# Kernel tuning notes

Hardware: AMD Instinct MI355X
Metric: run time of the kernel (lower is better)

## Reference

```python
import jax, jax.numpy as jnp
import numpy as np

N = 4096  # n == m: vector length and circulant size


def setup_inputs() -> dict:
    key = jax.random.key(0)
    ks = jax.random.split(key, 6)
    return {
        "key": jax.random.normal(ks[0], (N,), dtype=jnp.float32),
        "input_x": jax.random.normal(ks[1], (N,), dtype=jnp.float32),
        "key_matrix1": jax.random.normal(ks[2], (N, N), dtype=jnp.float32),
        "input_o1": jax.random.normal(ks[3], (N,), dtype=jnp.float32),
        "key_matrix2": jax.random.normal(ks[4], (N, N), dtype=jnp.float32),
        "input_o2": jax.random.normal(ks[5], (N,), dtype=jnp.float32),
    }


def reference(key, input_x, key_matrix1, input_o1, key_matrix2, input_o2):
    # Original loop: key_current_j[k] = key[(k - j) % m]  (a rolled copy of key),
    # result[j] = dot(key_current_j, input_x), then per-j correction:
    #   redun1 = (km1 @ key_current_j)[j]
    #   redun2 = sum_{i != j} (km1 @ key_current_j)[i] * input_o1[i]
    # and likewise redun3/redun4 with km2/input_o2; finally
    #   result[j] = (result[j] - redun2 - redun4) / redun1, returning (result, last redun3).
    n = input_x.shape[0]
    m = key.shape[0]
    # Circulant gather: K[j, k] = key[(k - j) % m], shape (n, m)
    idx = (jnp.arange(m)[None, :] - jnp.arange(n)[:, None]) % m
    K = key[idx]

    base = K @ input_x                                   # result before correction, (n,)

    # Diagonals of R = K @ km.T without forming R: d[j] = dot(K[j], km[j])
    d1 = jnp.einsum("jk,jk->j", K, key_matrix1)          # redun1 per j
    d2 = jnp.einsum("jk,jk->j", K, key_matrix2)          # redun3 per j

    # R @ o = (K @ km.T) @ o = K @ (km.T @ o): O(n^2) instead of O(n^3)
    r2 = K @ (key_matrix1.T @ input_o1) - d1 * input_o1  # redun2 per j (index j excluded)
    r4 = K @ (key_matrix2.T @ input_o2) - d2 * input_o2  # redun4 per j

    result = (base - r2 - r4) / d1
    redun3 = d2[-1]  # value from the last loop iteration j = n-1
    return result, redun3
```

## Files before the change

### kernel.cpp

```cpp
#include <hip/hip_runtime.h>

#define N 4096
#define MASK 4095

__device__ __forceinline__ float fold(float u, float v, int m) {
    const bool hi = (threadIdx.x & m) != 0;
    const float t = hi ? u : v;
    const float s = __shfl_xor(t, m, 64);
    return (hi ? v : u) + s;
}

__device__ __forceinline__ float greduce4(float g0, float g1, float g2, float g3) {
    float c1 = fold(g0, g1, 32);
    float c2 = fold(g2, g3, 32);
    float e  = fold(c1, c2, 16);
    e += __shfl_xor(e, 8, 64);
    e += __shfl_xor(e, 4, 64);
    e += __shfl_xor(e, 2, 64);
    e += __shfl_xor(e, 1, 64);
    return e;
}

__global__ __launch_bounds__(256) void k1_fused(
    const float* __restrict__ key,
    const float* __restrict__ km1, const float* __restrict__ km2,
    const float* __restrict__ o1, const float* __restrict__ o2,
    float* __restrict__ tpart1, float* __restrict__ tpart2,
    float* __restrict__ dpart1, float* __restrict__ dpart2)
{
    __shared__ float skey[544];
    const int t = threadIdx.x;
    const int b = blockIdx.x;
    const int rc = b >> 3;
    const int cc = b & 7;
    const int j0 = rc * 16;
    const int c0 = cc * 512;
    const int base = c0 - j0 - 15;

    for (int i = t; i < 527; i += 256)
        skey[i + (i >> 5)] = key[(base + i) & MASK];
    __syncthreads();

    float w[17];
    #pragma unroll
    for (int c = 0; c < 17; ++c) {
        const int idx = 2 * t + c;
        w[c] = skey[idx + (idx >> 5)];
    }

    const float2* q1 = (const float2*)(km1 + (size_t)j0 * N + c0);
    const float2* q2 = (const float2*)(km2 + (size_t)j0 * N + c0);

    float2 La[2][4], Lb[2][4];
    #pragma unroll
    for (int i = 0; i < 4; ++i) La[0][i] = q1[(size_t)i * 2048 + t];
    #pragma unroll
    for (int i = 0; i < 4; ++i) Lb[0][i] = q2[(size_t)i * 2048 + t];

    float tp1x = 0.f, tp1y = 0.f, tp2x = 0.f, tp2y = 0.f;
    float rd1[4], rd2[4];

    #pragma unroll
    for (int rb = 0; rb < 4; ++rb) {
        const int cur = rb & 1, nxt = cur ^ 1;
        if (rb < 3) {
            #pragma unroll
            for (int i = 0; i < 4; ++i) La[nxt][i] = q1[(size_t)((rb + 1) * 4 + i) * 2048 + t];
            #pragma unroll
            for (int i = 0; i < 4; ++i) Lb[nxt][i] = q2[(size_t)((rb + 1) * 4 + i) * 2048 + t];
        }
        float dpa[4], dpb[4];
        #pragma unroll
        for (int rr = 0; rr < 4; ++rr) {
            const int r = rb * 4 + rr;
            const float k0 = w[15 - r], k1v = w[16 - r];
            dpa[rr] = k0 * La[cur][rr].x + k1v * La[cur][rr].y;
            dpb[rr] = k0 * Lb[cur][rr].x + k1v * Lb[cur][rr].y;
            const float oa = o1[j0 + r], ob = o2[j0 + r];
            tp1x += oa * La[cur][rr].x; tp1y += oa * La[cur][rr].y;
            tp2x += ob * Lb[cur][rr].x; tp2y += ob * Lb[cur][rr].y;
        }
        rd1[rb] = greduce4(dpa[0], dpa[1], dpa[2], dpa[3]);
        rd2[rb] = greduce4(dpb[0], dpb[1], dpb[2], dpb[3]);
    }

    const int lane = t & 63, wave = t >> 6, sg = lane >> 4;
    const int off = (0x3120 >> (sg * 4)) & 0xF;
    if ((lane & 15) == 0) {
        #pragma unroll
        for (int qq = 0; qq < 4; ++qq) {
            dpart1[(size_t)(j0 + 4 * qq + off) * 32 + cc * 4 + wave] = rd1[qq];
            dpart2[(size_t)(j0 + 4 * qq + off) * 32 + cc * 4 + wave] = rd2[qq];
        }
    }

    ((float2*)(tpart1 + (size_t)rc * N + c0))[t] = make_float2(tp1x, tp1y);
    ((float2*)(tpart2 + (size_t)rc * N + c0))[t] = make_float2(tp2x, tp2y);
}

__global__ __launch_bounds__(256) void k2_reduce(
    const float* __restrict__ tpart1, const float* __restrict__ tpart2,
    const float* __restrict__ dpart1, const float* __restrict__ dpart2,
    float* __restrict__ t1, float* __restrict__ t2,
    float* __restrict__ d1, float* __restrict__ d2)
{
    __shared__ float sdata[256];
    const int b = blockIdx.x;
    const int t = threadIdx.x;

    if (b < 256) {
        const float* src = (b < 128) ? tpart1 : tpart2;
        float* dst       = (b < 128) ? t1 : t2;
        const int colbase = (b & 127) * 32;
        const int col = t & 31;
        const int sg = t >> 5;
        float a0 = 0.f, a1 = 0.f, a2 = 0.f, a3 = 0.f;
        #pragma unroll 4
        for (int k = 0; k < 32; k += 4) {
            a0 += src[(size_t)(sg + 8 * (k + 0)) * N + colbase + col];
            a1 += src[(size_t)(sg + 8 * (k + 1)) * N + colbase + col];
            a2 += src[(size_t)(sg + 8 * (k + 2)) * N + colbase + col];
            a3 += src[(size_t)(sg + 8 * (k + 3)) * N + colbase + col];
        }
        sdata[t] = (a0 + a1) + (a2 + a3);
        __syncthreads();
        if (t < 32) {
            float s = 0.f;
            #pragma unroll
            for (int i = 0; i < 8; ++i) s += sdata[i * 32 + t];
            dst[colbase + t] = s;
        }
    } else {
        const int db = b - 256;
        const float* src = (db < 512) ? dpart1 : dpart2;
        float* dst       = (db < 512) ? d1 : d2;
        const int rowbase = (db & 511) * 8;
        const int row = rowbase + (t >> 5);
        const int s = t & 31;
        float v = src[(size_t)row * 32 + s];
        #pragma unroll
        for (int off = 16; off > 0; off >>= 1) v += __shfl_down(v, off, 32);
        if (s == 0) dst[row] = v;
    }
}

__global__ __launch_bounds__(256) void k3_final(
    const float* __restrict__ key, const float* __restrict__ x,
    const float* __restrict__ t1, const float* __restrict__ t2,
    const float* __restrict__ d1, const float* __restrict__ d2,
    const float* __restrict__ o1, const float* __restrict__ o2,
    float* __restrict__ out)
{
    __shared__ float skey[4096 + 128];
    __shared__ float sred[48];
    const int t = threadIdx.x;
    const int j0 = blockIdx.x * 4;

    #pragma unroll
    for (int q = 0; q < 16; ++q) {
        const int idx = q * 256 + t;
        skey[idx + (idx >> 5)] = key[idx];
    }
    __syncthreads();

    float acc[4][3];
    #pragma unroll
    for (int r = 0; r < 4; ++r)
        #pragma unroll
        for (int v = 0; v < 3; ++v) acc[r][v] = 0.f;

    #pragma unroll
    for (int q = 0; q < 4; ++q) {
        const int k0 = q * 1024 + 4 * t;
        const float4 xv = *(const float4*)(x + k0);
        const float4 u1 = *(const float4*)(t1 + k0);
        const float4 u2 = *(const float4*)(t2 + k0);
        float kw[7];
        #pragma unroll
        for (int i = 0; i < 7; ++i) {
            const int widx = (k0 - j0 - 3 + i) & MASK;
            kw[i] = skey[widx + (widx >> 5)];
        }
        #pragma unroll
        for (int r = 0; r < 4; ++r) {
            const float kv0 = kw[3 - r], kv1 = kw[4 - r], kv2 = kw[5 - r], kv3 = kw[6 - r];
            acc[r][0] += kv0 * xv.x + kv1 * xv.y + kv2 * xv.z + kv3 * xv.w;
            acc[r][1] += kv0 * u1.x + kv1 * u1.y + kv2 * u1.z + kv3 * u1.w;
            acc[r][2] += kv0 * u2.x + kv1 * u2.y + kv2 * u2.z + kv3 * u2.w;
        }
    }

    float rv[3];
    #pragma unroll
    for (int v = 0; v < 3; ++v)
        rv[v] = greduce4(acc[0][v], acc[1][v], acc[2][v], acc[3][v]);

    const int lane = t & 63, wave = t >> 6, sg = lane >> 4;
    const int off = (0x3120 >> (sg * 4)) & 0xF;
    if ((lane & 15) == 0) {
        #pragma unroll
        for (int v = 0; v < 3; ++v) sred[wave * 12 + v * 4 + off] = rv[v];
    }
    __syncthreads();

    if (t < 4) {
        const int j = j0 + t;
        float vb = 0.f, v1 = 0.f, v2 = 0.f;
        #pragma unroll
        for (int wv = 0; wv < 4; ++wv) {
            vb += sred[wv * 12 + 0 + t];
            v1 += sred[wv * 12 + 4 + t];
            v2 += sred[wv * 12 + 8 + t];
        }
        const float dd1 = d1[j], dd2 = d2[j];
        const float r2 = v1 - dd1 * o1[j];
        const float r4 = v2 - dd2 * o2[j];
        out[j] = (vb - r2 - r4) / dd1;
        if (j == N - 1) out[N] = dd2;
    }
}

extern "C" void kernel_launch(void* const* d_in, const int* in_sizes, int n_in,
                              void* d_out, int out_size, void* d_ws, size_t ws_size,
                              hipStream_t stream) {
    const float* key = (const float*)d_in[0];
    const float* x   = (const float*)d_in[1];
    const float* km1 = (const float*)d_in[2];
    const float* o1  = (const float*)d_in[3];
    const float* km2 = (const float*)d_in[4];
    const float* o2  = (const float*)d_in[5];
    float* out = (float*)d_out;

    float* ws = (float*)d_ws;
    float* tpart1 = ws;
    float* tpart2 = tpart1 + (size_t)256 * N;
    float* dpart1 = tpart2 + (size_t)256 * N;
    float* dpart2 = dpart1 + (size_t)N * 32;
    float* t1     = dpart2 + (size_t)N * 32;
    float* t2     = t1 + N;
    float* d1     = t2 + N;
    float* d2     = d1 + N;

    hipLaunchKernelGGL(k1_fused, dim3(2048), dim3(256), 0, stream,
                       key, km1, km2, o1, o2, tpart1, tpart2, dpart1, dpart2);
    hipLaunchKernelGGL(k2_reduce, dim3(1280), dim3(256), 0, stream,
                       tpart1, tpart2, dpart1, dpart2, t1, t2, d1, d2);
    hipLaunchKernelGGL(k3_final, dim3(1024), dim3(256), 0, stream,
                       key, x, t1, t2, d1, d2, o1, o2, out);
}
```

Before: 35.27 us.

## Give each k1 block full rows with 1024 threads and float4 loads

The first kernel now launches 256 blocks of 1024 threads. Each block covers 16 full rows of both matrices using float4 loads, replacing 2048 blocks of 256 threads that each handled a 16x512 tile. The full key vector is staged in shared memory per block, and the per-row diagonal dot products are reduced with a 32-lane xor shuffle, writing 32 partials per row so the layout matches the existing reduce kernel. This widens memory transactions and cuts the block count, but uses fewer blocks on a large GPU, issues more shuffles per row, and adds a bigger shared-memory load per block.

```diff
diff --git a/kernel.cpp b/kernel.cpp
--- a/kernel.cpp
+++ b/kernel.cpp
@@ -2,6 +2,15 @@
 
 #define N 4096
 #define MASK 4095
+
+__device__ __forceinline__ float red32(float v) {
+    v += __shfl_xor(v, 1, 64);
+    v += __shfl_xor(v, 2, 64);
+    v += __shfl_xor(v, 4, 64);
+    v += __shfl_xor(v, 8, 64);
+    v += __shfl_xor(v, 16, 64);
+    return v;
+}
 
 __device__ __forceinline__ float fold(float u, float v, int m) {
     const bool hi = (threadIdx.x & m) != 0;
@@ -21,81 +30,74 @@
     return e;
 }
 
-__global__ __launch_bounds__(256) void k1_fused(
+__global__ __launch_bounds__(1024, 4) void k1_fused(
     const float* __restrict__ key,
     const float* __restrict__ km1, const float* __restrict__ km2,
     const float* __restrict__ o1, const float* __restrict__ o2,
     float* __restrict__ tpart1, float* __restrict__ tpart2,
     float* __restrict__ dpart1, float* __restrict__ dpart2)
 {
-    __shared__ float skey[544];
+    __shared__ float skey[4096 + 128];
     const int t = threadIdx.x;
     const int b = blockIdx.x;
-    const int rc = b >> 3;
-    const int cc = b & 7;
-    const int j0 = rc * 16;
-    const int c0 = cc * 512;
-    const int base = c0 - j0 - 15;
-
-    for (int i = t; i < 527; i += 256)
-        skey[i + (i >> 5)] = key[(base + i) & MASK];
+    const int j0 = b * 16;
+
+    #pragma unroll
+    for (int q = 0; q < 4; ++q) {
+        const int idx = q * 1024 + t;
+        skey[idx + (idx >> 5)] = key[idx];
+    }
     __syncthreads();
 
-    float w[17];
-    #pragma unroll
-    for (int c = 0; c < 17; ++c) {
-        const int idx = 2 * t + c;
-        w[c] = skey[idx + (idx >> 5)];
-    }
-
-    const float2* q1 = (const float2*)(km1 + (size_t)j0 * N + c0);
-    const float2* q2 = (const float2*)(km2 + (size_t)j0 * N + c0);
-
-    float2 La[2][4], Lb[2][4];
-    #pragma unroll
-    for (int i = 0; i < 4; ++i) La[0][i] = q1[(size_t)i * 2048 + t];
-    #pragma unroll
-    for (int i = 0; i < 4; ++i) Lb[0][i] = q2[(size_t)i * 2048 + t];
-
-    float tp1x = 0.f, tp1y = 0.f, tp2x = 0.f, tp2y = 0.f;
-    float rd1[4], rd2[4];
+    float w[19];
+    #pragma unroll
+    for (int i = 0; i < 19; ++i) {
+        const int idx = (4 * t - j0 - 15 + i) & MASK;
+        w[i] = skey[idx + (idx >> 5)];
+    }
+
+    const float4* q1 = (const float4*)km1 + (size_t)j0 * 1024 + t;
+    const float4* q2 = (const float4*)km2 + (size_t)j0 * 1024 + t;
+
+    float4 A[2][4], B[2][4];
+    #pragma unroll
+    for (int i = 0; i < 4; ++i) A[0][i] = q1[(size_t)i * 1024];
+    #pragma unroll
+    for (int i = 0; i < 4; ++i) B[0][i] = q2[(size_t)i * 1024];
+
+    float tp1[4] = {0.f, 0.f, 0.f, 0.f};
+    float tp2[4] = {0.f, 0.f, 0.f, 0.f};
 
     #pragma unroll
     for (int rb = 0; rb < 4; ++rb) {
         const int cur = rb & 1, nxt = cur ^ 1;
         if (rb < 3) {
             #pragma unroll
-            for (int i = 0; i < 4; ++i) La[nxt][i] = q1[(size_t)((rb + 1) * 4 + i) * 2048 + t];
+            for (int i = 0; i < 4; ++i) A[nxt][i] = q1[(size_t)((rb + 1) * 4 + i) * 1024];
             #pragma unroll
-            for (int i = 0; i < 4; ++i) Lb[nxt][i] = q2[(size_t)((rb + 1) * 4 + i) * 2048 + t];
-        }
-        float dpa[4], dpb[4];
+            for (int i = 0; i < 4; ++i) B[nxt][i] = q2[(size_t)((rb + 1) * 4 + i) * 1024];
+        }
         #pragma unroll
         for (int rr = 0; rr < 4; ++rr) {
             const int r = rb * 4 + rr;
-            const float k0 = w[15 - r], k1v = w[16 - r];
-            dpa[rr] = k0 * La[cur][rr].x + k1v * La[cur][rr].y;
-            dpb[rr] = k0 * Lb[cur][rr].x + k1v * Lb[cur][rr].y;
+            const float4 a = A[cur][rr];
+            const float4 v = B[cur][rr];
             const float oa = o1[j0 + r], ob = o2[j0 + r];
-            tp1x += oa * La[cur][rr].x; tp1y += oa * La[cur][rr].y;
-            tp2x += ob * Lb[cur][rr].x; tp2y += ob * Lb[cur][rr].y;
-        }
-        rd1[rb] = greduce4(dpa[0], dpa[1], dpa[2], dpa[3]);
-        rd2[rb] = greduce4(dpb[0], dpb[1], dpb[2], dpb[3]);
-    }
-
-    const int lane = t & 63, wave = t >> 6, sg = lane >> 4;
-    const int off = (0x3120 >> (sg * 4)) & 0xF;
-    if ((lane & 15) == 0) {
-        #pragma unroll
-        for (int qq = 0; qq < 4; ++qq) {
-            dpart1[(size_t)(j0 + 4 * qq + off) * 32 + cc * 4 + wave] = rd1[qq];
-            dpart2[(size_t)(j0 + 4 * qq + off) * 32 + cc * 4 + wave] = rd2[qq];
-        }
-    }
-
-    ((float2*)(tpart1 + (size_t)rc * N + c0))[t] = make_float2(tp1x, tp1y);
-    ((float2*)(tpart2 + (size_t)rc * N + c0))[t] = make_float2(tp2x, tp2y);
+            tp1[0] += oa * a.x; tp1[1] += oa * a.y; tp1[2] += oa * a.z; tp1[3] += oa * a.w;
+            tp2[0] += ob * v.x; tp2[1] += ob * v.y; tp2[2] += ob * v.z; tp2[3] += ob * v.w;
+            float dp1 = w[15 - r] * a.x + w[16 - r] * a.y + w[17 - r] * a.z + w[18 - r] * a.w;
+            float dp2 = w[15 - r] * v.x + w[16 - r] * v.y + w[17 - r] * v.z + w[18 - r] * v.w;
+            dp1 = red32(dp1);
+            dp2 = red32(dp2);
+            if ((t & 31) == 0) {
+                dpart1[(size_t)(j0 + r) * 32 + (t >> 5)] = dp1;
+                dpart2[(size_t)(j0 + r) * 32 + (t >> 5)] = dp2;
+            }
+        }
+    }
+
+    ((float4*)(tpart1 + (size_t)b * N))[t] = make_float4(tp1[0], tp1[1], tp1[2], tp1[3]);
+    ((float4*)(tpart2 + (size_t)b * N))[t] = make_float4(tp2[0], tp2[1], tp2[2], tp2[3]);
 }
 
 __global__ __launch_bounds__(256) void k2_reduce(
@@ -241,7 +243,7 @@
     float* d1     = t2 + N;
     float* d2     = d1 + N;
 
-    hipLaunchKernelGGL(k1_fused, dim3(2048), dim3(256), 0, stream,
+    hipLaunchKernelGGL(k1_fused, dim3(256), dim3(1024), 0, stream,
                        key, km1, km2, o1, o2, tpart1, tpart2, dpart1, dpart2);
     hipLaunchKernelGGL(k2_reduce, dim3(1280), dim3(256), 0, stream,
                        tpart1, tpart2, dpart1, dpart2, t1, t2, d1, d2);
```

New measurement: 47.23 us. 1.34x slower.
